# Kernel optimization log

Measured on AMD Instinct MI355X. Metric: run time of the kernel, lower is better.

The kernel has to match this reference:

```python
import jax, jax.numpy as jnp
import numpy as np

N_NODES = 50000
N_EDGES = 800000
EMB = 128
HID = [128, 128]
OUT = 64
CE = 8  # stand-in for CROSS_ENTROPY_INDEXES: first 8 output columns get sigmoid


def _linear_params(key, d_in, d_out):
    k1, k2 = jax.random.split(key)
    s = 1.0 / np.sqrt(d_in)
    w = jax.random.uniform(k1, (d_in, d_out), minval=-s, maxval=s, dtype=jnp.float32)
    b = jax.random.uniform(k2, (d_out,), minval=-s, maxval=s, dtype=jnp.float32)
    return w, b


def setup_inputs() -> dict:
    key = jax.random.key(0)
    ks = jax.random.split(key, 16)
    z = jax.random.normal(ks[0], (N_NODES, EMB), dtype=jnp.float32)
    edge_index = jax.random.randint(ks[1], (2, N_EDGES), 0, N_NODES, dtype=jnp.int64)
    # SAGEConv params: neighbor weight (with bias) + root weight
    w1_n, b1 = _linear_params(ks[2], EMB, HID[0])
    w1_r, _ = _linear_params(ks[3], EMB, HID[0])
    w2_n, b2 = _linear_params(ks[4], HID[0], HID[1])
    w2_r, _ = _linear_params(ks[5], HID[0], HID[1])
    wf_n, bf = _linear_params(ks[6], HID[1], OUT)
    wf_r, _ = _linear_params(ks[7], HID[1], OUT)
    # initial residual linears: emb -> hid[1], emb -> out
    w_res1, b_res1 = _linear_params(ks[8], EMB, HID[1])
    w_res2, b_res2 = _linear_params(ks[9], EMB, OUT)
    return dict(z=z, edge_index=edge_index,
                w1_n=w1_n, w1_r=w1_r, b1=b1,
                w2_n=w2_n, w2_r=w2_r, b2=b2,
                wf_n=wf_n, wf_r=wf_r, bf=bf,
                w_res1=w_res1, b_res1=b_res1,
                w_res2=w_res2, b_res2=b_res2)


def _sage(x, src, dst, w_n, w_r, b, n_nodes):
    # mean-aggregate neighbor features at target nodes, then affine combine with root
    msg = x[src]                                        # [E, d]
    agg = jax.ops.segment_sum(msg, dst, num_segments=n_nodes)
    deg = jax.ops.segment_sum(jnp.ones_like(dst, dtype=x.dtype), dst, num_segments=n_nodes)
    mean = agg / jnp.maximum(deg, 1.0)[:, None]
    return mean @ w_n + x @ w_r + b


def reference(z, edge_index, w1_n, w1_r, b1, w2_n, w2_r, b2, wf_n, wf_r, bf,
              w_res1, b_res1, w_res2, b_res2):
    n = z.shape[0]
    src, dst = edge_index[0], edge_index[1]
    h = jax.nn.relu(_sage(z, src, dst, w1_n, w1_r, b1, n))
    # mid layer (dropout is identity in eval) + initial residual
    h = jax.nn.relu(_sage(h, src, dst, w2_n, w2_r, b2, n))
    h = h + (z @ w_res1 + b_res1)
    # final conv + final residual
    h = _sage(h, src, dst, wf_n, wf_r, bf, n)
    h = h + (z @ w_res2 + b_res2)
    # sigmoid on cross-entropy columns
    h = h.at[:, :CE].set(jax.nn.sigmoid(h[:, :CE]))
    return h
```

## Files before the change

### kernel.cpp

```cpp
#include <hip/hip_runtime.h>
#include <hip/hip_bf16.h>
#include <math.h>

#define NN 50000
#define NE 800000
#define NB 391
#define EPB 6250

typedef short bf16x8 __attribute__((ext_vector_type(8)));
typedef float f32x4 __attribute__((ext_vector_type(4)));
typedef unsigned short us4 __attribute__((ext_vector_type(4)));
typedef unsigned short us8 __attribute__((ext_vector_type(8)));
typedef unsigned int u32x4 __attribute__((ext_vector_type(4)));

__device__ __forceinline__ float bf2f(unsigned short u) {
  union { unsigned int i; float f; } x; x.i = ((unsigned int)u) << 16; return x.f;
}
__device__ __forceinline__ unsigned short f2bf(float f) {
  union { float f; unsigned int i; } x; x.f = f;
  unsigned int i = x.i;
  unsigned int r = i + 0x7FFF + ((i >> 16) & 1);
  return (unsigned short)(r >> 16);
}
__device__ __forceinline__ us4 pack4(f32x4 v) {
  us4 o; o[0] = f2bf(v[0]); o[1] = f2bf(v[1]); o[2] = f2bf(v[2]); o[3] = f2bf(v[3]);
  return o;
}

__global__ __launch_bounds__(512) void bscan_kernel(const int* __restrict__ bhist,
                                                    int* __restrict__ bucket_off,
                                                    int* __restrict__ gcur) {
  __shared__ int s[512];
  int t = threadIdx.x;
  int v = (t < NB) ? bhist[t] : 0;
  s[t] = v; __syncthreads();
  for (int off = 1; off < 512; off <<= 1) {
    int x = (t >= off) ? s[t - off] : 0;
    __syncthreads();
    s[t] += x;
    __syncthreads();
  }
  if (t < NB) { bucket_off[t] = s[t] - v; gcur[t] = 0; }
  if (t == NB - 1) bucket_off[NB] = s[t];
}

__global__ __launch_bounds__(256) void bscat_kernel(const int* __restrict__ srcn,
                                                    const int* __restrict__ dstn,
                                                    const int* __restrict__ bucket_off,
                                                    int* __restrict__ gcur,
                                                    unsigned long long* __restrict__ ebuf) {
  __shared__ int hist[NB];
  __shared__ int base[NB];
  for (int i = threadIdx.x; i < NB; i += 256) hist[i] = 0;
  __syncthreads();
  int e0 = blockIdx.x * EPB;
  for (int i = threadIdx.x; i < EPB; i += 256)
    atomicAdd(&hist[dstn[e0 + i] >> 7], 1);
  __syncthreads();
  for (int i = threadIdx.x; i < NB; i += 256) {
    int c = hist[i];
    base[i] = c ? (bucket_off[i] + atomicAdd(&gcur[i], c)) : 0;
  }
  __syncthreads();
  for (int i = threadIdx.x; i < EPB; i += 256) {
    int s = srcn[e0 + i], d = dstn[e0 + i];
    int b = d >> 7;
    int pos = atomicSub(&hist[b], 1) - 1;
    unsigned long long e = ((unsigned long long)(unsigned)d << 32) | (unsigned)s;
    __builtin_nontemporal_store(e, &ebuf[(size_t)base[b] + pos]);
  }
}

__global__ __launch_bounds__(256) void bfill_kernel(const unsigned long long* __restrict__ ebuf,
                                                    const int* __restrict__ bucket_off,
                                                    int* __restrict__ rowoff,
                                                    int* __restrict__ csr) {
  int b = blockIdx.x;
  int bo = bucket_off[b], cnt = bucket_off[b + 1] - bo;
  __shared__ int ndeg[128], noff[128];
  int t = threadIdx.x;
  if (t < 128) ndeg[t] = 0;
  __syncthreads();
  for (int i = t; i < cnt; i += 256)
    atomicAdd(&ndeg[(int)(ebuf[bo + i] >> 32) & 127], 1);
  __syncthreads();
  if (t < 128) noff[t] = ndeg[t];
  __syncthreads();
  for (int off = 1; off < 128; off <<= 1) {
    int x = 0;
    if (t < 128 && t >= off) x = noff[t - off];
    __syncthreads();
    if (t < 128 && t >= off) noff[t] += x;
    __syncthreads();
  }
  if (t < 128) {
    int ex = noff[t] - ndeg[t];
    noff[t] = ex;
    int node = b * 128 + t;
    if (node < NN) rowoff[node] = bo + ex;
  }
  if (b == NB - 1 && t == 0) rowoff[NN] = NE;
  __syncthreads();
  for (int i = t; i < cnt; i += 256) {
    unsigned long long e = ebuf[bo + i];
    int dl = (int)(e >> 32) & 127;
    int pos = atomicSub(&ndeg[dl], 1) - 1;
    __builtin_nontemporal_store((int)(unsigned)e, &csr[bo + noff[dl] + pos]);
  }
}

__global__ __launch_bounds__(256) void setup_kernel(
    const float* __restrict__ z, unsigned short* __restrict__ A1,
    const float* __restrict__ w1n, const float* __restrict__ w1r,
    const float* __restrict__ w2n, const float* __restrict__ w2r,
    const float* __restrict__ wfn, const float* __restrict__ wfr,
    const float* __restrict__ wr1, const float* __restrict__ wr2,
    unsigned short* __restrict__ Bp1, unsigned short* __restrict__ Bp2,
    unsigned short* __restrict__ Bp3,
    const int* __restrict__ dstn, int* __restrict__ bhist) {
  __shared__ int h[NB];
  int b = blockIdx.x;
  if (b < 6250) {
    int i = b * 256 + threadIdx.x;
    if (i >= NN * 128 / 4) return;
    int i4 = i * 4;
    int row = i4 >> 7, c = i4 & 127;
    f32x4 v = *(const f32x4*)(z + i4);
    us4 o = { f2bf(v[0]), f2bf(v[1]), f2bf(v[2]), f2bf(v[3]) };
    __builtin_nontemporal_store(o, (us4*)(A1 + (size_t)row * 256 + 128 + c));
  } else if (b < 6314) {
    int g = (b - 6250) * 256 + threadIdx.x;
    unsigned short* D; int NT, fi;
    int which;
    if      (g < 10240) { fi = g;         D = Bp1; NT = 20; which = 1; }
    else if (g < 14336) { fi = g - 10240; D = Bp2; NT = 8;  which = 2; }
    else if (g < 16384) { fi = g - 14336; D = Bp3; NT = 4;  which = 3; }
    else return;
    int lane = fi & 63, t = fi >> 6;
    int nt = t % NT, k0i = t / NT;
    int m = lane & 15, q = lane >> 4;
    int kb = k0i * 32 + q * 8;
    int n = nt * 16 + m;
    int hi = (kb >= 128);
    int k0_ = kb - (hi ? 128 : 0);
    const float* W = nullptr; int Nseg = 128; int nn = n;
    if (which == 1) {
      if (n < 128)      { W = hi ? w1r : w1n; nn = n; Nseg = 128; }
      else if (n < 256) { W = hi ? wr1 : nullptr; nn = n - 128; Nseg = 128; }
      else              { W = hi ? wr2 : nullptr; nn = n - 256; Nseg = 64; }
    } else if (which == 2) { W = hi ? w2r : w2n; Nseg = 128; }
    else                   { W = hi ? wfr : wfn; Nseg = 64; }
    unsigned short o[8];
#pragma unroll
    for (int j = 0; j < 8; j++)
      o[j] = W ? f2bf(W[(size_t)(k0_ + j) * Nseg + nn]) : (unsigned short)0;
    *(us8*)(D + (size_t)fi * 8) = *(const us8*)o;
  } else {
    for (int i = threadIdx.x; i < NB; i += 256) h[i] = 0;
    __syncthreads();
    int e0 = (b - 6314) * EPB;
    for (int i = threadIdx.x; i < EPB; i += 256)
      atomicAdd(&h[dstn[e0 + i] >> 7], 1);
    __syncthreads();
    for (int i = threadIdx.x; i < NB; i += 256)
      if (h[i]) atomicAdd(&bhist[i], h[i]);
  }
}

__global__ __launch_bounds__(256) void agg_kernel(const unsigned short* __restrict__ feat, int fstride,
                                                  unsigned short* __restrict__ outm, int ostride,
                                                  const int* __restrict__ rowoff,
                                                  const int* __restrict__ csr) {
  int wave = threadIdx.x >> 6, lane = threadIdx.x & 63;
  int node = blockIdx.x * 4 + wave;
  if (node >= NN) return;
  int beg = rowoff[node], end = rowoff[node + 1];
  int g = lane >> 4;
  int c = (lane & 15) << 3;
  float a[8];
#pragma unroll
  for (int i = 0; i < 8; i++) a[i] = 0.f;
  int e1 = end - 1;
  for (int j = beg + g; j < end; j += 16) {
    int j1 = (j + 4 < e1) ? j + 4 : e1;
    int j2 = (j + 8 < e1) ? j + 8 : e1;
    int j3 = (j + 12 < e1) ? j + 12 : e1;
    int s0 = csr[j], s1 = csr[j1], s2 = csr[j2], s3 = csr[j3];
    float w1 = (j + 4 < end) ? 1.f : 0.f;
    float w2 = (j + 8 < end) ? 1.f : 0.f;
    float w3 = (j + 12 < end) ? 1.f : 0.f;
    u32x4 v0 = *(const u32x4*)(feat + (size_t)s0 * fstride + c);
    u32x4 v1 = *(const u32x4*)(feat + (size_t)s1 * fstride + c);
    u32x4 v2 = *(const u32x4*)(feat + (size_t)s2 * fstride + c);
    u32x4 v3 = *(const u32x4*)(feat + (size_t)s3 * fstride + c);
#pragma unroll
    for (int i = 0; i < 4; i++) {
      float l0 = bf2f((unsigned short)(v0[i] & 0xffff));
      float h0 = bf2f((unsigned short)(v0[i] >> 16));
      l0 = fmaf(w1, bf2f((unsigned short)(v1[i] & 0xffff)), l0);
      h0 = fmaf(w1, bf2f((unsigned short)(v1[i] >> 16)), h0);
      l0 = fmaf(w2, bf2f((unsigned short)(v2[i] & 0xffff)), l0);
      h0 = fmaf(w2, bf2f((unsigned short)(v2[i] >> 16)), h0);
      l0 = fmaf(w3, bf2f((unsigned short)(v3[i] & 0xffff)), l0);
      h0 = fmaf(w3, bf2f((unsigned short)(v3[i] >> 16)), h0);
      a[2*i] += l0;
      a[2*i+1] += h0;
    }
  }
#pragma unroll
  for (int i = 0; i < 8; i++) {
    a[i] += __shfl_xor(a[i], 16, 64);
    a[i] += __shfl_xor(a[i], 32, 64);
  }
  if (g == 0) {
    float inv = 1.f / fmaxf((float)(end - beg), 1.f);
    u32x4 o;
#pragma unroll
    for (int i = 0; i < 4; i++)
      o[i] = ((unsigned int)f2bf(a[2*i+1] * inv) << 16) | f2bf(a[2*i] * inv);
    __builtin_nontemporal_store(o, (u32x4*)(outm + (size_t)node * ostride + c));
  }
}

__global__ __launch_bounds__(256) void gemm1_kernel(
    const unsigned short* __restrict__ A,
    const unsigned short* __restrict__ Bp,
    const float* __restrict__ b1, const float* __restrict__ br1, const float* __restrict__ br2,
    unsigned short* __restrict__ h1out,
    unsigned short* __restrict__ res1, unsigned short* __restrict__ res2)
{
  const int NT = 20, TILES = 5;
  __shared__ unsigned short Bs[TILES * 8 * 512];
  int tid = threadIdx.x;
  int wave = tid >> 6, lane = tid & 63;
  int ybase = blockIdx.x * TILES;
  int row0 = blockIdx.y * 128 + wave * 16;
  int m = lane & 15, q = lane >> 4;
  const unsigned short* arow0 = A + (size_t)(row0 + m) * 256 + q * 8;
  const unsigned short* arow1 = arow0 + 64 * 256;
  bf16x8 af0[8], af1[8];
#pragma unroll
  for (int k0i = 0; k0i < 8; ++k0i) {
    af0[k0i] = *(const bf16x8*)(arow0 + k0i * 32);
    af1[k0i] = *(const bf16x8*)(arow1 + k0i * 32);
  }
#pragma unroll
  for (int i = tid; i < TILES * 64 * 8; i += 256) {
    int k0i = i / (TILES * 64), r = i % (TILES * 64);
    *(us8*)(Bs + (size_t)k0i * TILES * 512 + (size_t)r * 8) =
        *(const us8*)(Bp + ((size_t)k0i * NT + ybase) * 512 + (size_t)r * 8);
  }
  __syncthreads();
  f32x4 acc[2][TILES];
#pragma unroll
  for (int h = 0; h < 2; h++)
#pragma unroll
    for (int i = 0; i < TILES; i++) acc[h][i] = (f32x4){0.f, 0.f, 0.f, 0.f};
#pragma unroll
  for (int k0i = 0; k0i < 8; ++k0i) {
    const unsigned short* bk = Bs + (size_t)k0i * TILES * 512 + lane * 8;
#pragma unroll
    for (int s = 0; s < TILES; ++s) {
      bf16x8 bfr = *(const bf16x8*)(bk + s * 512);
      acc[0][s] = __builtin_amdgcn_mfma_f32_16x16x32_bf16(bfr, af0[k0i], acc[0][s], 0, 0, 0);
      acc[1][s] = __builtin_amdgcn_mfma_f32_16x16x32_bf16(bfr, af1[k0i], acc[1][s], 0, 0, 0);
    }
  }
  int cb = q * 4;
#pragma unroll
  for (int h = 0; h < 2; h++) {
    int row = row0 + h * 64 + m;
    if (row >= NN) continue;
#pragma unroll
    for (int s = 0; s < TILES; ++s) {
      int nt = ybase + s;
      f32x4 v = acc[h][s];
      if (nt < 8) {
        int col = nt * 16 + cb;
        f32x4 bb = *(const f32x4*)(b1 + col);
        v[0] = fmaxf(v[0] + bb[0], 0.f); v[1] = fmaxf(v[1] + bb[1], 0.f);
        v[2] = fmaxf(v[2] + bb[2], 0.f); v[3] = fmaxf(v[3] + bb[3], 0.f);
        __builtin_nontemporal_store(pack4(v), (us4*)(h1out + (size_t)row * 256 + col));
      } else if (nt < 16) {
        int col = (nt - 8) * 16 + cb;
        f32x4 bb = *(const f32x4*)(br1 + col);
        v[0] += bb[0]; v[1] += bb[1]; v[2] += bb[2]; v[3] += bb[3];
        __builtin_nontemporal_store(pack4(v), (us4*)(res1 + (size_t)row * 128 + col));
      } else {
        int col = (nt - 16) * 16 + cb;
        f32x4 bb = *(const f32x4*)(br2 + col);
        v[0] += bb[0]; v[1] += bb[1]; v[2] += bb[2]; v[3] += bb[3];
        __builtin_nontemporal_store(pack4(v), (us4*)(res2 + (size_t)row * 64 + col));
      }
    }
  }
}

template <int NTT, int RPW>
__global__ __launch_bounds__(256) void gemm23_kernel(
    const unsigned short* __restrict__ A,
    const unsigned short* __restrict__ Bp,
    const float* __restrict__ bias,
    const unsigned short* __restrict__ res, int res_stride,
    unsigned short* __restrict__ out_bf,
    float* __restrict__ out_f, int of_stride,
    int relu, int sig8)
{
  const int TILES = 4;
  __shared__ unsigned short Bs[TILES * 8 * 512];
  int tid = threadIdx.x;
  int wave = tid >> 6, lane = tid & 63;
  int ybase = blockIdx.x * TILES;
  int row0 = blockIdx.y * (64 * RPW) + wave * 16;
  int m = lane & 15, q = lane >> 4;
  bf16x8 af[RPW][8];
#pragma unroll
  for (int h = 0; h < RPW; h++) {
    const unsigned short* arow = A + (size_t)(row0 + h * 64 + m) * 256 + q * 8;
#pragma unroll
    for (int k0i = 0; k0i < 8; ++k0i) af[h][k0i] = *(const bf16x8*)(arow + k0i * 32);
  }
#pragma unroll
  for (int i = tid; i < TILES * 64 * 8; i += 256) {
    int k0i = i / (TILES * 64), r = i % (TILES * 64);
    *(us8*)(Bs + (size_t)k0i * TILES * 512 + (size_t)r * 8) =
        *(const us8*)(Bp + ((size_t)k0i * NTT + ybase) * 512 + (size_t)r * 8);
  }
  __syncthreads();
  f32x4 acc[RPW][TILES];
#pragma unroll
  for (int h = 0; h < RPW; h++)
#pragma unroll
    for (int i = 0; i < TILES; i++) acc[h][i] = (f32x4){0.f, 0.f, 0.f, 0.f};
#pragma unroll
  for (int k0i = 0; k0i < 8; ++k0i) {
    const unsigned short* bk = Bs + (size_t)k0i * TILES * 512 + lane * 8;
#pragma unroll
    for (int s = 0; s < TILES; ++s) {
      bf16x8 bfr = *(const bf16x8*)(bk + s * 512);
#pragma unroll
      for (int h = 0; h < RPW; h++)
        acc[h][s] = __builtin_amdgcn_mfma_f32_16x16x32_bf16(bfr, af[h][k0i], acc[h][s], 0, 0, 0);
    }
  }
  int cb = q * 4;
#pragma unroll
  for (int h = 0; h < RPW; h++) {
    int row = row0 + h * 64 + m;
    if (row >= NN) continue;
#pragma unroll
    for (int s = 0; s < TILES; ++s) {
      int col = (ybase + s) * 16 + cb;
      f32x4 v = acc[h][s];
      f32x4 bb = *(const f32x4*)(bias + col);
      v[0] += bb[0]; v[1] += bb[1]; v[2] += bb[2]; v[3] += bb[3];
      if (relu) {
#pragma unroll
        for (int r = 0; r < 4; r++) v[r] = fmaxf(v[r], 0.f);
      }
      if (res) {
        us4 rv = *(const us4*)(res + (size_t)row * res_stride + col);
#pragma unroll
        for (int r = 0; r < 4; r++) v[r] += bf2f(rv[r]);
      }
      if (sig8 && col < 8) {
#pragma unroll
        for (int r = 0; r < 4; r++) v[r] = 1.f / (1.f + __expf(-v[r]));
      }
      if (out_bf)
        __builtin_nontemporal_store(pack4(v), (us4*)(out_bf + (size_t)row * 256 + col));
      if (out_f)
        __builtin_nontemporal_store(v, (f32x4*)(out_f + (size_t)row * of_stride + col));
    }
  }
}

extern "C" void kernel_launch(void* const* d_in, const int* in_sizes, int n_in,
                              void* d_out, int out_size, void* d_ws, size_t ws_size,
                              hipStream_t stream) {
  const float* z   = (const float*)d_in[0];
  const int*   edge = (const int*)d_in[1];
  const int*   srcn = edge;
  const int*   dstn = edge + NE;
  const float* w1n = (const float*)d_in[2];
  const float* w1r = (const float*)d_in[3];
  const float* b1  = (const float*)d_in[4];
  const float* w2n = (const float*)d_in[5];
  const float* w2r = (const float*)d_in[6];
  const float* b2  = (const float*)d_in[7];
  const float* wfn = (const float*)d_in[8];
  const float* wfr = (const float*)d_in[9];
  const float* bfb = (const float*)d_in[10];
  const float* wr1 = (const float*)d_in[11];
  const float* br1 = (const float*)d_in[12];
  const float* wr2 = (const float*)d_in[13];
  const float* br2 = (const float*)d_in[14];
  float* out = (float*)d_out;

  char* p = (char*)d_ws;
  auto alloc = [&](size_t bytes) { char* r = p; p += (bytes + 255) & ~255ull; return r; };
  int* rowoff = (int*)alloc((size_t)(NN + 1) * 4);
  int* bhist  = (int*)alloc((size_t)NB * 4);
  int* bucket_off = (int*)alloc((size_t)(NB + 1) * 4);
  int* gcur   = (int*)alloc((size_t)NB * 4);
  int* csr    = (int*)alloc((size_t)NE * 4);
  unsigned short* A1 = (unsigned short*)alloc((size_t)NN * 256 * 2);
  unsigned short* A2 = (unsigned short*)alloc((size_t)NN * 256 * 2);
  unsigned short* res1 = (unsigned short*)alloc((size_t)NN * 128 * 2);
  unsigned short* res2 = (unsigned short*)alloc((size_t)NN * 64 * 2);
  unsigned short* Bp1 = (unsigned short*)alloc(10240 * 8 * 2);
  unsigned short* Bp2 = (unsigned short*)alloc(4096 * 8 * 2);
  unsigned short* Bp3 = (unsigned short*)alloc(2048 * 8 * 2);
  unsigned short* A3 = A1;
  unsigned long long* ebuf = (unsigned long long*)res1;

  hipMemsetAsync(bhist, 0, (size_t)NB * 4, stream);
  setup_kernel<<<6442, 256, 0, stream>>>(z, A1, w1n, w1r, w2n, w2r, wfn, wfr, wr1, wr2,
                                         Bp1, Bp2, Bp3, dstn, bhist);
  bscan_kernel<<<1, 512, 0, stream>>>(bhist, bucket_off, gcur);
  bscat_kernel<<<128, 256, 0, stream>>>(srcn, dstn, bucket_off, gcur, ebuf);
  bfill_kernel<<<NB, 256, 0, stream>>>(ebuf, bucket_off, rowoff, csr);

  const int gy128 = (NN + 127) / 128;
  const int gy64  = (NN + 63) / 64;
  const int agg_blocks = (NN + 3) / 4;

  agg_kernel<<<agg_blocks, 256, 0, stream>>>(A1 + 128, 256, A1, 256, rowoff, csr);
  gemm1_kernel<<<dim3(4, gy128), 256, 0, stream>>>(A1, Bp1, b1, br1, br2, A2 + 128, res1, res2);

  agg_kernel<<<agg_blocks, 256, 0, stream>>>(A2 + 128, 256, A2, 256, rowoff, csr);
  gemm23_kernel<8, 2><<<dim3(2, gy128), 256, 0, stream>>>(A2, Bp2, b2, res1, 128,
      A3 + 128, nullptr, 0, 1, 0);

  agg_kernel<<<agg_blocks, 256, 0, stream>>>(A3 + 128, 256, A3, 256, rowoff, csr);
  gemm23_kernel<4, 1><<<dim3(1, gy64), 256, 0, stream>>>(A3, Bp3, bfb, res2, 64,
      nullptr, out, 64, 0, 1);
}
```

Before: 333.4 us.

## Gather from column-sliced feature copy in aggregation to improve cache locality

Producers now also write node features into a second buffer split into four 32-column slices, each stored contiguously per node. Aggregation launches a 2D grid with one slice per y-block, so each gather reads 64-byte rows from a 3.2MB slice that can stay in L2/MALL instead of 256-byte rows from the whole array. Nontemporal stores are also replaced with ordinary stores so the freshly written data can stay cached. The cost is an extra write of every feature matrix and four times as many aggregation passes over the CSR indices.

```diff
diff --git a/kernel.cpp b/kernel.cpp
--- a/kernel.cpp
+++ b/kernel.cpp
@@ -66,8 +66,7 @@
     int s = srcn[e0 + i], d = dstn[e0 + i];
     int b = d >> 7;
     int pos = atomicSub(&hist[b], 1) - 1;
-    unsigned long long e = ((unsigned long long)(unsigned)d << 32) | (unsigned)s;
-    __builtin_nontemporal_store(e, &ebuf[(size_t)base[b] + pos]);
+    ebuf[(size_t)base[b] + pos] = ((unsigned long long)(unsigned)d << 32) | (unsigned)s;
   }
 }
 
@@ -105,12 +104,13 @@
     unsigned long long e = ebuf[bo + i];
     int dl = (int)(e >> 32) & 127;
     int pos = atomicSub(&ndeg[dl], 1) - 1;
-    __builtin_nontemporal_store((int)(unsigned)e, &csr[bo + noff[dl] + pos]);
+    csr[bo + noff[dl] + pos] = (int)(unsigned)e;
   }
 }
 
 __global__ __launch_bounds__(256) void setup_kernel(
     const float* __restrict__ z, unsigned short* __restrict__ A1,
+    unsigned short* __restrict__ ts,
     const float* __restrict__ w1n, const float* __restrict__ w1r,
     const float* __restrict__ w2n, const float* __restrict__ w2r,
     const float* __restrict__ wfn, const float* __restrict__ wfr,
@@ -127,7 +127,8 @@
     int row = i4 >> 7, c = i4 & 127;
     f32x4 v = *(const f32x4*)(z + i4);
     us4 o = { f2bf(v[0]), f2bf(v[1]), f2bf(v[2]), f2bf(v[3]) };
-    __builtin_nontemporal_store(o, (us4*)(A1 + (size_t)row * 256 + 128 + c));
+    *(us4*)(A1 + (size_t)row * 256 + 128 + c) = o;
+    *(us4*)(ts + ((size_t)(c >> 5) * NN + row) * 32 + (c & 31)) = o;
   } else if (b < 6314) {
     int g = (b - 6250) * 256 + threadIdx.x;
     unsigned short* D; int NT, fi;
@@ -167,19 +168,19 @@
   }
 }
 
-__global__ __launch_bounds__(256) void agg_kernel(const unsigned short* __restrict__ feat, int fstride,
+__global__ __launch_bounds__(256) void agg_kernel(const unsigned short* __restrict__ ts,
                                                   unsigned short* __restrict__ outm, int ostride,
                                                   const int* __restrict__ rowoff,
                                                   const int* __restrict__ csr) {
+  int p = blockIdx.y;
+  const unsigned short* sl = ts + (size_t)p * NN * 32;
   int wave = threadIdx.x >> 6, lane = threadIdx.x & 63;
   int node = blockIdx.x * 4 + wave;
   if (node >= NN) return;
   int beg = rowoff[node], end = rowoff[node + 1];
   int g = lane >> 4;
-  int c = (lane & 15) << 3;
-  float a[8];
-#pragma unroll
-  for (int i = 0; i < 8; i++) a[i] = 0.f;
+  int c = (lane & 15) << 1;
+  float a0 = 0.f, a1 = 0.f;
   int e1 = end - 1;
   for (int j = beg + g; j < end; j += 16) {
     int j1 = (j + 4 < e1) ? j + 4 : e1;
@@ -189,36 +190,26 @@
     float w1 = (j + 4 < end) ? 1.f : 0.f;
     float w2 = (j + 8 < end) ? 1.f : 0.f;
     float w3 = (j + 12 < end) ? 1.f : 0.f;
-    u32x4 v0 = *(const u32x4*)(feat + (size_t)s0 * fstride + c);
-    u32x4 v1 = *(const u32x4*)(feat + (size_t)s1 * fstride + c);
-    u32x4 v2 = *(const u32x4*)(feat + (size_t)s2 * fstride + c);
-    u32x4 v3 = *(const u32x4*)(feat + (size_t)s3 * fstride + c);
-#pragma unroll
-    for (int i = 0; i < 4; i++) {
-      float l0 = bf2f((unsigned short)(v0[i] & 0xffff));
-      float h0 = bf2f((unsigned short)(v0[i] >> 16));
-      l0 = fmaf(w1, bf2f((unsigned short)(v1[i] & 0xffff)), l0);
-      h0 = fmaf(w1, bf2f((unsigned short)(v1[i] >> 16)), h0);
-      l0 = fmaf(w2, bf2f((unsigned short)(v2[i] & 0xffff)), l0);
-      h0 = fmaf(w2, bf2f((unsigned short)(v2[i] >> 16)), h0);
-      l0 = fmaf(w3, bf2f((unsigned short)(v3[i] & 0xffff)), l0);
-      h0 = fmaf(w3, bf2f((unsigned short)(v3[i] >> 16)), h0);
-      a[2*i] += l0;
-      a[2*i+1] += h0;
-    }
-  }
-#pragma unroll
-  for (int i = 0; i < 8; i++) {
-    a[i] += __shfl_xor(a[i], 16, 64);
-    a[i] += __shfl_xor(a[i], 32, 64);
-  }
+    unsigned int v0 = *(const unsigned int*)(sl + (size_t)s0 * 32 + c);
+    unsigned int v1 = *(const unsigned int*)(sl + (size_t)s1 * 32 + c);
+    unsigned int v2 = *(const unsigned int*)(sl + (size_t)s2 * 32 + c);
+    unsigned int v3 = *(const unsigned int*)(sl + (size_t)s3 * 32 + c);
+    float l0 = bf2f((unsigned short)(v0 & 0xffff));
+    float h0 = bf2f((unsigned short)(v0 >> 16));
+    l0 = fmaf(w1, bf2f((unsigned short)(v1 & 0xffff)), l0);
+    h0 = fmaf(w1, bf2f((unsigned short)(v1 >> 16)), h0);
+    l0 = fmaf(w2, bf2f((unsigned short)(v2 & 0xffff)), l0);
+    h0 = fmaf(w2, bf2f((unsigned short)(v2 >> 16)), h0);
+    l0 = fmaf(w3, bf2f((unsigned short)(v3 & 0xffff)), l0);
+    h0 = fmaf(w3, bf2f((unsigned short)(v3 >> 16)), h0);
+    a0 += l0; a1 += h0;
+  }
+  a0 += __shfl_xor(a0, 16, 64); a0 += __shfl_xor(a0, 32, 64);
+  a1 += __shfl_xor(a1, 16, 64); a1 += __shfl_xor(a1, 32, 64);
   if (g == 0) {
     float inv = 1.f / fmaxf((float)(end - beg), 1.f);
-    u32x4 o;
-#pragma unroll
-    for (int i = 0; i < 4; i++)
-      o[i] = ((unsigned int)f2bf(a[2*i+1] * inv) << 16) | f2bf(a[2*i] * inv);
-    __builtin_nontemporal_store(o, (u32x4*)(outm + (size_t)node * ostride + c));
+    unsigned int o = ((unsigned int)f2bf(a1 * inv) << 16) | f2bf(a0 * inv);
+    *(unsigned int*)(outm + (size_t)node * ostride + p * 32 + c) = o;
   }
 }
 
@@ -227,6 +218,7 @@
     const unsigned short* __restrict__ Bp,
     const float* __restrict__ b1, const float* __restrict__ br1, const float* __restrict__ br2,
     unsigned short* __restrict__ h1out,
+    unsigned short* __restrict__ ts,
     unsigned short* __restrict__ res1, unsigned short* __restrict__ res2)
 {
   const int NT = 20, TILES = 5;
@@ -280,17 +272,19 @@
         f32x4 bb = *(const f32x4*)(b1 + col);
         v[0] = fmaxf(v[0] + bb[0], 0.f); v[1] = fmaxf(v[1] + bb[1], 0.f);
         v[2] = fmaxf(v[2] + bb[2], 0.f); v[3] = fmaxf(v[3] + bb[3], 0.f);
-        __builtin_nontemporal_store(pack4(v), (us4*)(h1out + (size_t)row * 256 + col));
+        us4 pk = pack4(v);
+        *(us4*)(h1out + (size_t)row * 256 + col) = pk;
+        *(us4*)(ts + ((size_t)(col >> 5) * NN + row) * 32 + (col & 31)) = pk;
       } else if (nt < 16) {
         int col = (nt - 8) * 16 + cb;
         f32x4 bb = *(const f32x4*)(br1 + col);
         v[0] += bb[0]; v[1] += bb[1]; v[2] += bb[2]; v[3] += bb[3];
-        __builtin_nontemporal_store(pack4(v), (us4*)(res1 + (size_t)row * 128 + col));
+        *(us4*)(res1 + (size_t)row * 128 + col) = pack4(v);
       } else {
         int col = (nt - 16) * 16 + cb;
         f32x4 bb = *(const f32x4*)(br2 + col);
         v[0] += bb[0]; v[1] += bb[1]; v[2] += bb[2]; v[3] += bb[3];
-        __builtin_nontemporal_store(pack4(v), (us4*)(res2 + (size_t)row * 64 + col));
+        *(us4*)(res2 + (size_t)row * 64 + col) = pack4(v);
       }
     }
   }
@@ -303,6 +297,7 @@
     const float* __restrict__ bias,
     const unsigned short* __restrict__ res, int res_stride,
     unsigned short* __restrict__ out_bf,
+    unsigned short* __restrict__ ts,
     float* __restrict__ out_f, int of_stride,
     int relu, int sig8)
 {
@@ -367,10 +362,13 @@
 #pragma unroll
         for (int r = 0; r < 4; r++) v[r] = 1.f / (1.f + __expf(-v[r]));
       }
-      if (out_bf)
-        __builtin_nontemporal_store(pack4(v), (us4*)(out_bf + (size_t)row * 256 + col));
+      if (out_bf) {
+        us4 pk = pack4(v);
+        *(us4*)(out_bf + (size_t)row * 256 + col) = pk;
+        if (ts) *(us4*)(ts + ((size_t)(col >> 5) * NN + row) * 32 + (col & 31)) = pk;
+      }
       if (out_f)
-        __builtin_nontemporal_store(v, (f32x4*)(out_f + (size_t)row * of_stride + col));
+        *(f32x4*)(out_f + (size_t)row * of_stride + col) = v;
     }
   }
 }
@@ -406,6 +404,7 @@
   int* csr    = (int*)alloc((size_t)NE * 4);
   unsigned short* A1 = (unsigned short*)alloc((size_t)NN * 256 * 2);
   unsigned short* A2 = (unsigned short*)alloc((size_t)NN * 256 * 2);
+  unsigned short* ts = (unsigned short*)alloc((size_t)NN * 128 * 2);
   unsigned short* res1 = (unsigned short*)alloc((size_t)NN * 128 * 2);
   unsigned short* res2 = (unsigned short*)alloc((size_t)NN * 64 * 2);
   unsigned short* Bp1 = (unsigned short*)alloc(10240 * 8 * 2);
@@ -415,7 +414,7 @@
   unsigned long long* ebuf = (unsigned long long*)res1;
 
   hipMemsetAsync(bhist, 0, (size_t)NB * 4, stream);
-  setup_kernel<<<6442, 256, 0, stream>>>(z, A1, w1n, w1r, w2n, w2r, wfn, wfr, wr1, wr2,
+  setup_kernel<<<6442, 256, 0, stream>>>(z, A1, ts, w1n, w1r, w2n, w2r, wfn, wfr, wr1, wr2,
                                          Bp1, Bp2, Bp3, dstn, bhist);
   bscan_kernel<<<1, 512, 0, stream>>>(bhist, bucket_off, gcur);
   bscat_kernel<<<128, 256, 0, stream>>>(srcn, dstn, bucket_off, gcur, ebuf);
@@ -423,16 +422,17 @@
 
   const int gy128 = (NN + 127) / 128;
   const int gy64  = (NN + 63) / 64;
-  const int agg_blocks = (NN + 3) / 4;
-
-  agg_kernel<<<agg_blocks, 256, 0, stream>>>(A1 + 128, 256, A1, 256, rowoff, csr);
-  gemm1_kernel<<<dim3(4, gy128), 256, 0, stream>>>(A1, Bp1, b1, br1, br2, A2 + 128, res1, res2);
-
-  agg_kernel<<<agg_blocks, 256, 0, stream>>>(A2 + 128, 256, A2, 256, rowoff, csr);
+  const int aggx = (NN + 3) / 4;
+
+  agg_kernel<<<dim3(aggx, 4), 256, 0, stream>>>(ts, A1, 256, rowoff, csr);
+  gemm1_kernel<<<dim3(4, gy128), 256, 0, stream>>>(A1, Bp1, b1, br1, br2,
+      A2 + 128, ts, res1, res2);
+
+  agg_kernel<<<dim3(aggx, 4), 256, 0, stream>>>(ts, A2, 256, rowoff, csr);
   gemm23_kernel<8, 2><<<dim3(2, gy128), 256, 0, stream>>>(A2, Bp2, b2, res1, 128,
-      A3 + 128, nullptr, 0, 1, 0);
-
-  agg_kernel<<<agg_blocks, 256, 0, stream>>>(A3 + 128, 256, A3, 256, rowoff, csr);
+      A3 + 128, ts, nullptr, 0, 1, 0);
+
+  agg_kernel<<<dim3(aggx, 4), 256, 0, stream>>>(ts, A3, 256, rowoff, csr);
   gemm23_kernel<4, 1><<<dim3(1, gy64), 256, 0, stream>>>(A3, Bp3, bfb, res2, 64,
-      nullptr, out, 64, 0, 1);
-}
+      nullptr, nullptr, out, 64, 0, 1);
+}
```

Result: slower. 390.2 us (+17.0%).
